# Performance work log

Hardware: AMD Instinct MI355X
Metric: run time of the kernel (lower is better)

## Reference

```python
import jax, jax.numpy as jnp
import numpy as np


def setup_inputs() -> dict:
    key = jax.random.key(0)
    B, T, H, W = 32, 1024, 32, 32
    dim_s = 32
    # spike ids per (batch, time, h, w), values in [0, dim_s)
    inp = jax.random.randint(key, (B, T, H, W), 0, dim_s, dtype=jnp.int32)
    return {"input": inp, "dim_s": dim_s}


def reference(input, dim_s):
    # input: [B, T, H, W] int32 spike ids in [0, dim_s)
    # out:   [B, dim_s, H, W] int32 counts: out[b,s,h,w] = #{t : input[b,t,h,w]==s}
    B, T, H, W = input.shape
    b_idx = jnp.arange(B, dtype=jnp.int32)[:, None, None, None]   # [B,1,1,1]
    h_idx = jnp.arange(H, dtype=jnp.int32)[None, None, :, None]   # [1,1,H,1]
    w_idx = jnp.arange(W, dtype=jnp.int32)[None, None, None, :]   # [1,1,1,W]
    hist = jnp.zeros((B, dim_s, H, W), dtype=jnp.int32)
    # scatter-add one count per (b, t, h, w) into bin input[b,t,h,w]
    hist = hist.at[b_idx, input, h_idx, w_idx].add(jnp.int32(1))
    return hist
```

## Files before the change

### kernel.cpp

```cpp
#include <hip/hip_runtime.h>


constexpr int T_DIM   = 1024;
constexpr int HW      = 1024;
constexpr int DIM_S   = 32;
constexpr int PIX_PB  = 128;
constexpr int QUADS   = PIX_PB / 4;
constexpr int THREADS = 512;
constexpr int SLICES  = THREADS / QUADS;
constexpr int T_PER_THREAD = T_DIM / SLICES;
constexpr int CHUNKS  = HW / PIX_PB;

__global__ __launch_bounds__(THREADS) void spike_hist_kernel(
    const int* __restrict__ in, int* __restrict__ out) {
    __shared__ unsigned lds[32 * THREADS];

    const int tid  = threadIdx.x;
    const int quad = tid & (QUADS - 1);
    const int sl   = tid >> 5;
    const int blk  = blockIdx.x;
    const int b    = blk >> 3;
    const int pix0 = (blk & (CHUNKS - 1)) * PIX_PB;

    const int* __restrict__ base = in
        + (size_t)b * (T_DIM * HW)
        + (size_t)(sl * T_PER_THREAD) * HW
        + pix0 + quad * 4;

    unsigned cw[32];
    #pragma unroll
    for (int m = 0; m < 32; ++m) cw[m] = 0u;

    #pragma unroll
    for (int g = 0; g < 2; ++g) {
        unsigned pl[4][5];
        #pragma unroll
        for (int c = 0; c < 4; ++c)
            #pragma unroll
            for (int j = 0; j < 5; ++j) pl[c][j] = 0u;

        #pragma unroll
        for (int ph = 0; ph < 4; ++ph) {
            int4 v[8];
            #pragma unroll
            for (int i = 0; i < 8; ++i)
                v[i] = *(const int4*)(base + (size_t)(g * 32 + ph * 8 + i) * HW);
            #pragma unroll
            for (int i = 0; i < 8; ++i) {
                const int ti = ph * 8 + i;
                const unsigned xs[4] = { (unsigned)v[i].x, (unsigned)v[i].y,
                                         (unsigned)v[i].z, (unsigned)v[i].w };
                #pragma unroll
                for (int c = 0; c < 4; ++c) {
                    const unsigned x = xs[c];
                    #pragma unroll
                    for (int j = 0; j < 5; ++j)
                        pl[c][j] |= ((x >> j) & 1u) << ti;
                }
            }
        }

        #pragma unroll
        for (int c = 0; c < 4; ++c) {
            const unsigned p0 = pl[c][0], p1 = pl[c][1], p2 = pl[c][2],
                           p3 = pl[c][3], p4 = pl[c][4];
            const unsigned n0 = ~p0, n1 = ~p1, n2 = ~p2, n3 = ~p3, n4 = ~p4;
            const unsigned a[4]  = { n1 & n0, n1 & p0, p1 & n0, p1 & p0 };
            const unsigned bq[4] = { n3 & n2, n3 & p2, p3 & n2, p3 & p2 };
            #pragma unroll
            for (int j = 0; j < 4; ++j) {
                #pragma unroll
                for (int k = 0; k < 4; ++k) {
                    const unsigned ab = bq[j] & a[k];
                    cw[c * 8 + j]     += (unsigned)__builtin_popcount(ab & n4) << (k * 8);
                    cw[c * 8 + 4 + j] += (unsigned)__builtin_popcount(ab & p4) << (k * 8);
                }
            }
        }
    }

    #pragma unroll
    for (int m = 0; m < 32; ++m) lds[m * THREADS + tid] = cw[m];
    __syncthreads();

    int* __restrict__ outb = out + (size_t)b * (DIM_S * HW) + pix0;
    #pragma unroll
    for (int k = 0; k < 2; ++k) {
        const int col = k * THREADS + tid;
        const int q   = col & 31;
        const int m   = col >> 5;
        const int c   = m >> 3;
        const int w   = m & 7;
        unsigned lo = 0u, hi = 0u;
        #pragma unroll
        for (int s2 = 0; s2 < SLICES; ++s2) {
            const unsigned x = lds[m * THREADS + s2 * 32 + q];
            lo += x & 0x00FF00FFu;
            hi += (x >> 8) & 0x00FF00FFu;
        }
        const int s_base = (w >> 2) * 16 + (w & 3) * 4;
        const int px     = q * 4 + c;
        int* __restrict__ op = outb + (size_t)s_base * HW + px;
        op[0 * HW] = (int)(lo & 0xFFFFu);
        op[1 * HW] = (int)(hi & 0xFFFFu);
        op[2 * HW] = (int)(lo >> 16);
        op[3 * HW] = (int)(hi >> 16);
    }
}

extern "C" void kernel_launch(void* const* d_in, const int* in_sizes, int n_in,
                              void* d_out, int out_size, void* d_ws, size_t ws_size,
                              hipStream_t stream) {
    const int* in = (const int*)d_in[0];
    int* out      = (int*)d_out;
    const int B   = in_sizes[0] / (T_DIM * HW);
    const int grid = B * CHUNKS;
    spike_hist_kernel<<<grid, THREADS, 0, stream>>>(in, out);
}
```

Baseline: 192.6 us.

## Split histogram into per-slab partial kernel plus separate reduction kernel

```diff
diff --git a/kernel.cpp b/kernel.cpp
--- a/kernel.cpp
+++ b/kernel.cpp
@@ -4,103 +4,98 @@
 constexpr int T_DIM   = 1024;
 constexpr int HW      = 1024;
 constexpr int DIM_S   = 32;
-constexpr int PIX_PB  = 128;
-constexpr int QUADS   = PIX_PB / 4;
-constexpr int THREADS = 512;
-constexpr int SLICES  = THREADS / QUADS;
-constexpr int T_PER_THREAD = T_DIM / SLICES;
-constexpr int CHUNKS  = HW / PIX_PB;
+constexpr int SLAB_T  = 32;
+constexpr int STAGE_T = 16;
+constexpr int SLABS   = T_DIM / SLAB_T;
+constexpr int THREADS_A = 512;
+constexpr int THREADS_B = 256;
 
-__global__ __launch_bounds__(THREADS) void spike_hist_kernel(
-    const int* __restrict__ in, int* __restrict__ out) {
-    __shared__ unsigned lds[32 * THREADS];
+__global__ __launch_bounds__(THREADS_A) void spike_hist_partial(
+    const int* __restrict__ in, unsigned* __restrict__ ws) {
+    __shared__ int4 lds4[STAGE_T * HW / 4];
+    int* lds_i = (int*)lds4;
 
     const int tid  = threadIdx.x;
-    const int quad = tid & (QUADS - 1);
-    const int sl   = tid >> 5;
     const int blk  = blockIdx.x;
-    const int b    = blk >> 3;
-    const int pix0 = (blk & (CHUNKS - 1)) * PIX_PB;
+    const int b    = blk >> 5;
+    const int slab = blk & (SLABS - 1);
+    const size_t in_base = (size_t)(b * T_DIM + slab * SLAB_T) * HW;
 
-    const int* __restrict__ base = in
-        + (size_t)b * (T_DIM * HW)
-        + (size_t)(sl * T_PER_THREAD) * HW
-        + pix0 + quad * 4;
-
-    unsigned cw[32];
+    unsigned pl[2][5];
     #pragma unroll
-    for (int m = 0; m < 32; ++m) cw[m] = 0u;
+    for (int c = 0; c < 2; ++c)
+        #pragma unroll
+        for (int j = 0; j < 5; ++j) pl[c][j] = 0u;
 
     #pragma unroll
-    for (int g = 0; g < 2; ++g) {
-        unsigned pl[4][5];
+    for (int stage = 0; stage < 2; ++stage) {
+        if (stage) __syncthreads();
+        const int4* __restrict__ gsrc =
+            (const int4*)(in + in_base + (size_t)stage * STAGE_T * HW);
+        int4 v[8];
         #pragma unroll
-        for (int c = 0; c < 4; ++c)
-            #pragma unroll
-            for (int j = 0; j < 5; ++j) pl[c][j] = 0u;
+        for (int k = 0; k < 8; ++k) v[k] = gsrc[k * THREADS_A + tid];
+        #pragma unroll
+        for (int k = 0; k < 8; ++k) lds4[k * THREADS_A + tid] = v[k];
+        __syncthreads();
 
         #pragma unroll
-        for (int ph = 0; ph < 4; ++ph) {
-            int4 v[8];
+        for (int c = 0; c < 2; ++c) {
+            const int px = c * THREADS_A + tid;
             #pragma unroll
-            for (int i = 0; i < 8; ++i)
-                v[i] = *(const int4*)(base + (size_t)(g * 32 + ph * 8 + i) * HW);
-            #pragma unroll
-            for (int i = 0; i < 8; ++i) {
-                const int ti = ph * 8 + i;
-                const unsigned xs[4] = { (unsigned)v[i].x, (unsigned)v[i].y,
-                                         (unsigned)v[i].z, (unsigned)v[i].w };
+            for (int t = 0; t < STAGE_T; ++t) {
+                const unsigned x = (unsigned)lds_i[t * HW + px];
+                const int bit = stage * STAGE_T + t;
                 #pragma unroll
-                for (int c = 0; c < 4; ++c) {
-                    const unsigned x = xs[c];
-                    #pragma unroll
-                    for (int j = 0; j < 5; ++j)
-                        pl[c][j] |= ((x >> j) & 1u) << ti;
-                }
-            }
-        }
-
-        #pragma unroll
-        for (int c = 0; c < 4; ++c) {
-            const unsigned p0 = pl[c][0], p1 = pl[c][1], p2 = pl[c][2],
-                           p3 = pl[c][3], p4 = pl[c][4];
-            const unsigned n0 = ~p0, n1 = ~p1, n2 = ~p2, n3 = ~p3, n4 = ~p4;
-            const unsigned a[4]  = { n1 & n0, n1 & p0, p1 & n0, p1 & p0 };
-            const unsigned bq[4] = { n3 & n2, n3 & p2, p3 & n2, p3 & p2 };
-            #pragma unroll
-            for (int j = 0; j < 4; ++j) {
-                #pragma unroll
-                for (int k = 0; k < 4; ++k) {
-                    const unsigned ab = bq[j] & a[k];
-                    cw[c * 8 + j]     += (unsigned)__builtin_popcount(ab & n4) << (k * 8);
-                    cw[c * 8 + 4 + j] += (unsigned)__builtin_popcount(ab & p4) << (k * 8);
-                }
+                for (int j = 0; j < 5; ++j)
+                    pl[c][j] |= ((x >> j) & 1u) << bit;
             }
         }
     }
 
     #pragma unroll
-    for (int m = 0; m < 32; ++m) lds[m * THREADS + tid] = cw[m];
-    __syncthreads();
+    for (int c = 0; c < 2; ++c) {
+        const int px = c * THREADS_A + tid;
+        const unsigned p0 = pl[c][0], p1 = pl[c][1], p2 = pl[c][2],
+                       p3 = pl[c][3], p4 = pl[c][4];
+        const unsigned n0 = ~p0, n1 = ~p1, n2 = ~p2, n3 = ~p3;
+        const unsigned a[4]  = { n1 & n0, n1 & p0, p1 & n0, p1 & p0 };
+        const unsigned bq[4] = { n3 & n2, n3 & p2, p3 & n2, p3 & p2 };
+        #pragma unroll
+        for (int s4 = 0; s4 < 2; ++s4) {
+            const unsigned m4 = s4 ? p4 : ~p4;
+            #pragma unroll
+            for (int j = 0; j < 4; ++j) {
+                unsigned word = 0u;
+                #pragma unroll
+                for (int k = 0; k < 4; ++k)
+                    word |= (unsigned)__builtin_popcount(bq[j] & a[k] & m4)
+                            << (k * 8);
+                ws[((size_t)(b * SLABS + slab) * 8 + (s4 * 4 + j)) * HW + px]
+                    = word;
+            }
+        }
+    }
+}
 
-    int* __restrict__ outb = out + (size_t)b * (DIM_S * HW) + pix0;
+__global__ __launch_bounds__(THREADS_B) void spike_hist_reduce(
+    const unsigned* __restrict__ ws, int* __restrict__ out) {
+    const int blk = blockIdx.x;
+    const int b   = blk >> 3;
+    const int w   = blk & 7;
+    const int tid = threadIdx.x;
     #pragma unroll
-    for (int k = 0; k < 2; ++k) {
-        const int col = k * THREADS + tid;
-        const int q   = col & 31;
-        const int m   = col >> 5;
-        const int c   = m >> 3;
-        const int w   = m & 7;
+    for (int r = 0; r < 4; ++r) {
+        const int px = r * THREADS_B + tid;
         unsigned lo = 0u, hi = 0u;
         #pragma unroll
-        for (int s2 = 0; s2 < SLICES; ++s2) {
-            const unsigned x = lds[m * THREADS + s2 * 32 + q];
+        for (int slab = 0; slab < SLABS; ++slab) {
+            const unsigned x =
+                ws[((size_t)(b * SLABS + slab) * 8 + w) * HW + px];
             lo += x & 0x00FF00FFu;
             hi += (x >> 8) & 0x00FF00FFu;
         }
-        const int s_base = (w >> 2) * 16 + (w & 3) * 4;
-        const int px     = q * 4 + c;
-        int* __restrict__ op = outb + (size_t)s_base * HW + px;
+        int* __restrict__ op = out + ((size_t)b * DIM_S + w * 4) * HW + px;
         op[0 * HW] = (int)(lo & 0xFFFFu);
         op[1 * HW] = (int)(hi & 0xFFFFu);
         op[2 * HW] = (int)(lo >> 16);
@@ -113,7 +108,8 @@
                               hipStream_t stream) {
     const int* in = (const int*)d_in[0];
     int* out      = (int*)d_out;
+    unsigned* ws  = (unsigned*)d_ws;
     const int B   = in_sizes[0] / (T_DIM * HW);
-    const int grid = B * CHUNKS;
-    spike_hist_kernel<<<grid, THREADS, 0, stream>>>(in, out);
+    spike_hist_partial<<<B * SLABS, THREADS_A, 0, stream>>>(in, ws);
+    spike_hist_reduce <<<B * 8,     THREADS_B, 0, stream>>>(ws, out);
 }
```

After: 200.6 us. 4.2% more time.
